# Performance work log

Measured on AMD Instinct MI355X. Metric: run time of the kernel, lower is better.

The kernel has to match this reference:

```python
import jax, jax.numpy as jnp
import numpy as np

N_NODES = 50000
N_EDGES = 800000
N_FEAT = 512
N_HEADS = 8
OUT_PER_HEAD = 32  # nhid // nheads = 256 // 8
ALPHA = 0.2  # LeakyReLU negative slope


def setup_inputs() -> dict:
    key = jax.random.key(0)
    ks = jax.random.split(key, 7)
    h = jax.random.normal(ks[0], (N_NODES, N_FEAT), dtype=jnp.float32)
    src = jax.random.randint(ks[1], (N_EDGES,), 0, N_NODES)
    dst = jax.random.randint(ks[2], (N_EDGES,), 0, N_NODES)
    # per-head linear W: [H, F, O], bias [H, O]; attention vector a: [H, 2O], bias [H]
    W = jax.random.normal(ks[3], (N_HEADS, N_FEAT, OUT_PER_HEAD), dtype=jnp.float32) * 0.05
    Wb = jax.random.normal(ks[4], (N_HEADS, OUT_PER_HEAD), dtype=jnp.float32) * 0.05
    a = jax.random.normal(ks[5], (N_HEADS, 2 * OUT_PER_HEAD), dtype=jnp.float32) * 0.05
    ab = jax.random.normal(ks[6], (N_HEADS,), dtype=jnp.float32) * 0.05
    return {"h": h, "src": src, "dst": dst, "W": W, "Wb": Wb, "a": a, "ab": ab}


def reference(h, src, dst, W, Wb, a, ab):
    N = h.shape[0]
    H, F_in, O = W.shape
    # Per-head projection Wh = W(h): [N, H, O]
    Wh = jnp.einsum('nf,hfo->nho', h, W) + Wb
    # a @ concat(Wh_src, Wh_dst) == a_src @ Wh_src + a_dst @ Wh_dst
    a_src, a_dst = a[:, :O], a[:, O:]
    e_s = jnp.einsum('nho,ho->nh', Wh, a_src)  # [N, H]
    e_d = jnp.einsum('nho,ho->nh', Wh, a_dst)
    e = e_s[src] + e_d[dst] + ab               # [E, H]
    e = jnp.where(e > 0, e, ALPHA * e)         # LeakyReLU
    # Segment softmax over incoming edges of each destination node
    m = jax.ops.segment_max(e, dst, num_segments=N)        # [N, H]
    m = jnp.where(jnp.isfinite(m), m, jnp.zeros_like(m))   # isolated nodes
    w = jnp.exp(e - m[dst])                                # [E, H]
    denom = jax.ops.segment_sum(w, dst, num_segments=N)    # [N, H]
    att = w / jnp.where(denom[dst] > 0, denom[dst], 1.0)   # [E, H]
    # Weighted aggregation of source projections, per head, then concat heads
    out = jax.ops.segment_sum(att[:, :, None] * Wh[src], dst, num_segments=N)  # [N, H, O]
    return out.reshape(N, H * O)
```

## Files before the change

### kernel.cpp

```cpp
#include <hip/hip_runtime.h>
#include <math.h>

#define ALPHA 0.2f
#define CAP 64

constexpr int F_IN  = 512;
constexpr int HO    = 256;
constexpr int NHEAD = 8;

using bf16x8 = __attribute__((ext_vector_type(8))) short;
using bf16x4 = __attribute__((ext_vector_type(4))) short;
using f32x4  = __attribute__((ext_vector_type(4))) float;

__device__ __forceinline__ ushort f2bf(float f) {
    uint u = __float_as_uint(f);
    uint r = (u + 0x7FFFu + ((u >> 16) & 1u)) >> 16;
    return (ushort)r;
}
__device__ __forceinline__ float bf2f(ushort b) {
    return __uint_as_float(((uint)b) << 16);
}

__global__ __launch_bounds__(256) void prep_kernel(const float* __restrict__ W,
                                                   ushort* __restrict__ Wf,
                                                   const int* __restrict__ dst,
                                                   int* __restrict__ cnt,
                                                   int* __restrict__ rnk, int E) {
    const int bid = blockIdx.x;
    const int t = threadIdx.x;
    if (bid < 64) {
        int g = bid * 256 + t;
        int l   = g & 63;
        int oct = (g >> 6) & 15;
        int ks  = g >> 10;
        int oc  = oct * 16 + (l & 15);
        int hh  = oc >> 5, oo = oc & 31;
        int kb  = ks * 32 + (l >> 4) * 8;
        ushort v[8];
#pragma unroll
        for (int j = 0; j < 8; ++j)
            v[j] = f2bf(W[((size_t)hh * F_IN + kb + j) * 32 + oo]);
        bf16x8 o = { (short)v[0], (short)v[1], (short)v[2], (short)v[3],
                     (short)v[4], (short)v[5], (short)v[6], (short)v[7] };
        *(bf16x8*)(Wf + (size_t)g * 8) = o;
    } else {
        int base = (bid - 64) * 1024;
#pragma unroll
        for (int q = 0; q < 4; ++q) {
            int i = base + q * 256 + t;
            if (i < E) rnk[i] = atomicAdd(&cnt[dst[i]], 1);
        }
    }
}

__global__ __launch_bounds__(256) void scan1_kernel(const int* __restrict__ cnt,
                                                    int* __restrict__ bsum, int N) {
    __shared__ int red[256];
    const int t = threadIdx.x;
    const int b0 = blockIdx.x * 1024;
    int s = 0;
#pragma unroll
    for (int q = 0; q < 4; ++q) {
        int i = b0 + t * 4 + q;
        if (i < N) s += cnt[i];
    }
    red[t] = s;
    __syncthreads();
    for (int st = 128; st > 0; st >>= 1) {
        if (t < st) red[t] += red[t + st];
        __syncthreads();
    }
    if (t == 0) bsum[blockIdx.x] = red[0];
}

__global__ __launch_bounds__(64) void scan2_kernel(int* __restrict__ bsum, int nblk) {
    int l = threadIdx.x;
    int x = (l < nblk) ? bsum[l] : 0;
    int inc = x;
    for (int d = 1; d < 64; d <<= 1) {
        int v = __shfl_up(inc, d);
        if (l >= d) inc += v;
    }
    if (l < nblk) bsum[l] = inc - x;
}

__global__ __launch_bounds__(256) void scan3_kernel(const int* __restrict__ cnt,
                                                    const int* __restrict__ bsum,
                                                    int* __restrict__ off, int N, int E) {
    __shared__ int part[256];
    const int t = threadIdx.x;
    const int b0 = blockIdx.x * 1024;
    int v[4];
    int s = 0;
#pragma unroll
    for (int q = 0; q < 4; ++q) {
        int i = b0 + t * 4 + q;
        v[q] = (i < N) ? cnt[i] : 0;
        s += v[q];
    }
    part[t] = s;
    __syncthreads();
    for (int d = 1; d < 256; d <<= 1) {
        int x = (t >= d) ? part[t - d] : 0;
        __syncthreads();
        part[t] += x;
        __syncthreads();
    }
    int run = bsum[blockIdx.x] + ((t == 0) ? 0 : part[t - 1]);
#pragma unroll
    for (int q = 0; q < 4; ++q) {
        int i = b0 + t * 4 + q;
        if (i < N) { off[i] = run; run += v[q]; }
    }
    if (blockIdx.x == 0 && t == 0) off[N] = E;
}

__global__ __launch_bounds__(256) void place_kernel(const int* __restrict__ src,
                                                    const int* __restrict__ dst,
                                                    const int* __restrict__ rnk,
                                                    const int* __restrict__ off,
                                                    int* __restrict__ se, int E) {
    int base = blockIdx.x * 1024;
#pragma unroll
    for (int q = 0; q < 4; ++q) {
        int i = base + q * 256 + threadIdx.x;
        if (i < E) se[off[dst[i]] + rnk[i]] = src[i];
    }
}

__global__ __launch_bounds__(256, 2) void gemm_kernel(
    const float* __restrict__ h, const ushort* __restrict__ Wf,
    const float* __restrict__ Wb, const float* __restrict__ a,
    ushort* __restrict__ Wh, float* __restrict__ es, float* __restrict__ ed, int N)
{
    __shared__ ushort hs[2][128 * 40];
    const int t = threadIdx.x;
    const int l = t & 63;
    const int w = t >> 6;
    const int l15 = l & 15, l4 = l >> 4;
    const int n0 = blockIdx.x * 128;

    const int sr = t >> 1;
    const int sc = (t & 1) * 16;
    int srow = n0 + sr; if (srow >= N) srow = N - 1;
    const float* hrow = h + (size_t)srow * F_IN + sc;

    f32x4 acc[4][8];
#pragma unroll
    for (int i = 0; i < 4; ++i)
#pragma unroll
        for (int nt = 0; nt < 8; ++nt) acc[i][nt] = (f32x4){0.f, 0.f, 0.f, 0.f};

    {
        float4 v0 = *(const float4*)(hrow);
        float4 v1 = *(const float4*)(hrow + 4);
        float4 v2 = *(const float4*)(hrow + 8);
        float4 v3 = *(const float4*)(hrow + 12);
        bf16x8 o0 = { (short)f2bf(v0.x), (short)f2bf(v0.y), (short)f2bf(v0.z), (short)f2bf(v0.w),
                      (short)f2bf(v1.x), (short)f2bf(v1.y), (short)f2bf(v1.z), (short)f2bf(v1.w) };
        bf16x8 o1 = { (short)f2bf(v2.x), (short)f2bf(v2.y), (short)f2bf(v2.z), (short)f2bf(v2.w),
                      (short)f2bf(v3.x), (short)f2bf(v3.y), (short)f2bf(v3.z), (short)f2bf(v3.w) };
        *(bf16x8*)&hs[0][sr * 40 + sc]     = o0;
        *(bf16x8*)&hs[0][sr * 40 + sc + 8] = o1;
    }
    __syncthreads();

    for (int ks = 0; ks < 16; ++ks) {
        const int cb = ks & 1;
        float4 nx0, nx1, nx2, nx3;
        if (ks < 15) {
            const float* p = hrow + (ks + 1) * 32;
            nx0 = *(const float4*)(p);
            nx1 = *(const float4*)(p + 4);
            nx2 = *(const float4*)(p + 8);
            nx3 = *(const float4*)(p + 12);
        }
        bf16x8 af[4];
#pragma unroll
        for (int i = 0; i < 4; ++i)
            af[i] = *(const bf16x8*)(Wf + ((size_t)((ks * 16 + 4 * w + i) * 64 + l)) * 8);
#pragma unroll
        for (int half = 0; half < 2; ++half) {
            bf16x8 b4[4];
#pragma unroll
            for (int j = 0; j < 4; ++j)
                b4[j] = *(const bf16x8*)&hs[cb][((half * 4 + j) * 16 + l15) * 40 + l4 * 8];
#pragma unroll
            for (int i = 0; i < 4; ++i)
#pragma unroll
                for (int j = 0; j < 4; ++j)
                    acc[i][half * 4 + j] = __builtin_amdgcn_mfma_f32_16x16x32_bf16(
                        af[i], b4[j], acc[i][half * 4 + j], 0, 0, 0);
        }
        if (ks < 15) {
            bf16x8 o0 = { (short)f2bf(nx0.x), (short)f2bf(nx0.y), (short)f2bf(nx0.z), (short)f2bf(nx0.w),
                          (short)f2bf(nx1.x), (short)f2bf(nx1.y), (short)f2bf(nx1.z), (short)f2bf(nx1.w) };
            bf16x8 o1 = { (short)f2bf(nx2.x), (short)f2bf(nx2.y), (short)f2bf(nx2.z), (short)f2bf(nx2.w),
                          (short)f2bf(nx3.x), (short)f2bf(nx3.y), (short)f2bf(nx3.z), (short)f2bf(nx3.w) };
            *(bf16x8*)&hs[cb ^ 1][sr * 40 + sc]     = o0;
            *(bf16x8*)&hs[cb ^ 1][sr * 40 + sc + 8] = o1;
            __syncthreads();
        }
    }

    float4 wb4[4], as4[4], ad4[4];
    int ocb[4];
#pragma unroll
    for (int i = 0; i < 4; ++i) {
        int oc_base = (4 * w + i) * 16 + (l4 << 2);
        ocb[i] = oc_base;
        int head = oc_base >> 5;
        wb4[i] = *(const float4*)(Wb + oc_base);
        as4[i] = *(const float4*)(a + head * 64 + (oc_base & 31));
        ad4[i] = *(const float4*)(a + head * 64 + 32 + (oc_base & 31));
    }
#pragma unroll
    for (int nt = 0; nt < 8; ++nt) {
        int node = n0 + nt * 16 + l15;
        bool ok = node < N;
        float pe[4] = {0.f, 0.f, 0.f, 0.f};
#pragma unroll
        for (int i = 0; i < 4; ++i) {
            f32x4 v = acc[i][nt];
            float r0 = v.x + wb4[i].x, r1 = v.y + wb4[i].y;
            float r2 = v.z + wb4[i].z, r3 = v.w + wb4[i].w;
            if (ok) {
                bf16x4 o = { (short)f2bf(r0), (short)f2bf(r1), (short)f2bf(r2), (short)f2bf(r3) };
                *(bf16x4*)(Wh + (size_t)node * HO + ocb[i]) = o;
            }
            float dsv = r0 * as4[i].x + r1 * as4[i].y + r2 * as4[i].z + r3 * as4[i].w;
            float ddv = r0 * ad4[i].x + r1 * ad4[i].y + r2 * ad4[i].z + r3 * ad4[i].w;
            int hp = i >> 1;
            pe[hp] += dsv; pe[2 + hp] += ddv;
        }
#pragma unroll
        for (int q = 0; q < 4; ++q) {
            pe[q] += __shfl_xor(pe[q], 16);
            pe[q] += __shfl_xor(pe[q], 32);
        }
        if (l4 == 0 && ok) {
            es[(size_t)node * NHEAD + 2 * w]     = pe[0];
            es[(size_t)node * NHEAD + 2 * w + 1] = pe[1];
            ed[(size_t)node * NHEAD + 2 * w]     = pe[2];
            ed[(size_t)node * NHEAD + 2 * w + 1] = pe[3];
        }
    }
}

__global__ __launch_bounds__(256) void node_kernel(
    const int* __restrict__ se, const int* __restrict__ off,
    const float* __restrict__ es, const float* __restrict__ ed,
    const float* __restrict__ ab, const ushort* __restrict__ Wh,
    float* __restrict__ out, int N)
{
    __shared__ float wbuf[4][CAP][NHEAD];
    __shared__ int   sbuf[4][CAP];
    __shared__ float dinv[4][NHEAD];

    const int t = threadIdx.x;
    const int l = t & 63;
    const int wv = t >> 6;
    const int n = blockIdx.x * 4 + wv;
    const bool active = n < N;

    int beg = 0, deg = 0;
    if (active) { beg = off[n]; deg = off[n + 1] - beg; }

    const int slot = l >> 3, hh = l & 7;
    float edn = 0.f, abh = 0.f;
    if (active && deg > 0) {
        edn = ed[(size_t)n * NHEAD + hh];
        abh = ab[hh];
    }

    float dloc = 0.f;
    for (int j = slot; j < deg; j += 8) {
        int s = se[beg + j];
        float ev = es[(size_t)s * NHEAD + hh] + edn + abh;
        ev = ev > 0.f ? ev : ALPHA * ev;
        float wj = __expf(ev);
        if (j < CAP) {
            wbuf[wv][j][hh] = wj;
            if (hh == 0) sbuf[wv][j] = s;
        }
        dloc += wj;
    }
    dloc += __shfl_xor(dloc, 8);
    dloc += __shfl_xor(dloc, 16);
    dloc += __shfl_xor(dloc, 32);
    if (slot == 0) dinv[wv][hh] = (dloc > 0.f) ? 1.f / dloc : 1.f;
    __syncthreads();

    const int oc0 = (l & 31) * 8;
    const int hb  = oc0 >> 5;
    const int par = l >> 5;
    float acc[8] = {0.f, 0.f, 0.f, 0.f, 0.f, 0.f, 0.f, 0.f};

    if (active) {
        const int dcap = deg < CAP ? deg : CAP;
        int j = par;
        for (; j + 6 < dcap; j += 8) {
            int s0 = sbuf[wv][j];
            int s1 = sbuf[wv][j + 2];
            int s2 = sbuf[wv][j + 4];
            int s3 = sbuf[wv][j + 6];
            float w0 = wbuf[wv][j][hb];
            float w1 = wbuf[wv][j + 2][hb];
            float w2 = wbuf[wv][j + 4][hb];
            float w3 = wbuf[wv][j + 6][hb];
            bf16x8 r0 = *(const bf16x8*)(Wh + (size_t)s0 * HO + oc0);
            bf16x8 r1 = *(const bf16x8*)(Wh + (size_t)s1 * HO + oc0);
            bf16x8 r2 = *(const bf16x8*)(Wh + (size_t)s2 * HO + oc0);
            bf16x8 r3 = *(const bf16x8*)(Wh + (size_t)s3 * HO + oc0);
#pragma unroll
            for (int i = 0; i < 8; ++i) acc[i] += w0 * bf2f((ushort)r0[i]);
#pragma unroll
            for (int i = 0; i < 8; ++i) acc[i] += w1 * bf2f((ushort)r1[i]);
#pragma unroll
            for (int i = 0; i < 8; ++i) acc[i] += w2 * bf2f((ushort)r2[i]);
#pragma unroll
            for (int i = 0; i < 8; ++i) acc[i] += w3 * bf2f((ushort)r3[i]);
        }
        for (; j < dcap; j += 2) {
            int s = sbuf[wv][j];
            float wj = wbuf[wv][j][hb];
            bf16x8 row = *(const bf16x8*)(Wh + (size_t)s * HO + oc0);
#pragma unroll
            for (int i = 0; i < 8; ++i)
                acc[i] += wj * bf2f((ushort)row[i]);
        }
        if (deg > CAP) {
            float edb = ed[(size_t)n * NHEAD + hb] + ab[hb];
            for (int j2 = CAP + par; j2 < deg; j2 += 2) {
                int s = se[beg + j2];
                float ev = es[(size_t)s * NHEAD + hb] + edb;
                ev = ev > 0.f ? ev : ALPHA * ev;
                float wj = __expf(ev);
                bf16x8 row = *(const bf16x8*)(Wh + (size_t)s * HO + oc0);
#pragma unroll
                for (int i = 0; i < 8; ++i)
                    acc[i] += wj * bf2f((ushort)row[i]);
            }
        }
    }
#pragma unroll
    for (int i = 0; i < 8; ++i) acc[i] += __shfl_xor(acc[i], 32);

    if (active && par == 0) {
        float inv = dinv[wv][hb];
        float4 o0 = make_float4(acc[0] * inv, acc[1] * inv, acc[2] * inv, acc[3] * inv);
        float4 o1 = make_float4(acc[4] * inv, acc[5] * inv, acc[6] * inv, acc[7] * inv);
        *(float4*)(out + (size_t)n * HO + oc0)     = o0;
        *(float4*)(out + (size_t)n * HO + oc0 + 4) = o1;
    }
}

extern "C" void kernel_launch(void* const* d_in, const int* in_sizes, int n_in,
                              void* d_out, int out_size, void* d_ws, size_t ws_size,
                              hipStream_t stream) {
    const float* h   = (const float*)d_in[0];
    const int*   src = (const int*)  d_in[1];
    const int*   dst = (const int*)  d_in[2];
    const float* W   = (const float*)d_in[3];
    const float* Wb  = (const float*)d_in[4];
    const float* a   = (const float*)d_in[5];
    const float* ab  = (const float*)d_in[6];
    float* out = (float*)d_out;

    const int N = in_sizes[0] / F_IN;
    const int E = in_sizes[1];

    auto align_up = [](size_t x) { return (x + 255) & ~size_t(255); };
    char* p = (char*)d_ws;
    ushort* Wh = (ushort*)p; p += align_up((size_t)N * HO * 2);
    float*  es = (float*)p;  p += align_up((size_t)N * NHEAD * 4);
    float*  ed = (float*)p;  p += align_up((size_t)N * NHEAD * 4);
    int* cnt   = (int*)p;    p += align_up((size_t)N * 4);
    int* off   = (int*)p;    p += align_up((size_t)(N + 1) * 4);
    int* rnk   = (int*)p;    p += align_up((size_t)E * 4);
    int* se    = (int*)p;    p += align_up((size_t)E * 4);
    int* bsum  = (int*)p;    p += align_up((size_t)64 * 4);
    ushort* Wf = (ushort*)p; p += align_up((size_t)16 * 16 * 64 * 8 * 2);

    const int nblk = (N + 1023) / 1024;
    const int EB   = (E + 1023) / 1024;
    const int GB   = (N + 127) / 128;

    hipMemsetAsync(cnt, 0, (size_t)N * sizeof(int), stream);
    prep_kernel<<<64 + EB, 256, 0, stream>>>(W, Wf, dst, cnt, rnk, E);
    scan1_kernel<<<nblk, 256, 0, stream>>>(cnt, bsum, N);
    scan2_kernel<<<1, 64, 0, stream>>>(bsum, nblk);
    scan3_kernel<<<nblk, 256, 0, stream>>>(cnt, bsum, off, N, E);
    place_kernel<<<EB, 256, 0, stream>>>(src, dst, rnk, off, se, E);
    gemm_kernel<<<GB, 256, 0, stream>>>(h, Wf, Wb, a, Wh, es, ed, N);
    node_kernel<<<(N + 3) / 4, 256, 0, stream>>>(se, off, es, ed, ab, Wh, out, N);
}
```

Baseline: 164.2 us.

## Sort destination nodes by in-degree so node kernel blocks are balanced

Builds a counting sort of nodes by in-degree (capped at 63) inside the existing scan kernels, using per-block histograms and a prefix over buckets. The result is a permutation that the node kernel uses to map waves to nodes, so the four waves in a block handle nodes of similar degree and fewer waves sit idle waiting on a long neighbour. It adds histogram atomics, one more scan step and an extra indirection per node. It also loses the locality of output writes, since consecutive waves no longer write adjacent rows.

```diff
diff --git a/kernel.cpp b/kernel.cpp
--- a/kernel.cpp
+++ b/kernel.cpp
@@ -7,6 +7,7 @@
 constexpr int F_IN  = 512;
 constexpr int HO    = 256;
 constexpr int NHEAD = 8;
+constexpr int MAXBLK = 64;
 
 using bf16x8 = __attribute__((ext_vector_type(8))) short;
 using bf16x4 = __attribute__((ext_vector_type(4))) short;
@@ -54,15 +55,24 @@
 }
 
 __global__ __launch_bounds__(256) void scan1_kernel(const int* __restrict__ cnt,
-                                                    int* __restrict__ bsum, int N) {
+                                                    int* __restrict__ bsum,
+                                                    int* __restrict__ bh,
+                                                    int N, int nblk) {
     __shared__ int red[256];
+    __shared__ int hb[64];
     const int t = threadIdx.x;
     const int b0 = blockIdx.x * 1024;
+    if (t < 64) hb[t] = 0;
+    __syncthreads();
     int s = 0;
 #pragma unroll
     for (int q = 0; q < 4; ++q) {
         int i = b0 + t * 4 + q;
-        if (i < N) s += cnt[i];
+        if (i < N) {
+            int v = cnt[i];
+            s += v;
+            atomicAdd(&hb[v > 63 ? 63 : v], 1);
+        }
     }
     red[t] = s;
     __syncthreads();
@@ -71,25 +81,50 @@
         __syncthreads();
     }
     if (t == 0) bsum[blockIdx.x] = red[0];
-}
-
-__global__ __launch_bounds__(64) void scan2_kernel(int* __restrict__ bsum, int nblk) {
-    int l = threadIdx.x;
-    int x = (l < nblk) ? bsum[l] : 0;
-    int inc = x;
-    for (int d = 1; d < 64; d <<= 1) {
-        int v = __shfl_up(inc, d);
-        if (l >= d) inc += v;
-    }
-    if (l < nblk) bsum[l] = inc - x;
+    if (t < 64) bh[t * nblk + blockIdx.x] = hb[t];
+}
+
+__global__ __launch_bounds__(128) void scan2_kernel(int* __restrict__ bsum, int nblk,
+                                                    const int* __restrict__ bh,
+                                                    int* __restrict__ obb) {
+    int t = threadIdx.x;
+    if (t < 64) {
+        int l = t;
+        int x = (l < nblk) ? bsum[l] : 0;
+        int inc = x;
+        for (int d = 1; d < 64; d <<= 1) {
+            int v = __shfl_up(inc, d);
+            if (l >= d) inc += v;
+        }
+        if (l < nblk) bsum[l] = inc - x;
+    } else {
+        int b = t - 64;
+        int tot = 0;
+        for (int k = 0; k < nblk; ++k) tot += bh[b * nblk + k];
+        int inc = tot;
+        for (int d = 1; d < 64; d <<= 1) {
+            int v = __shfl_up(inc, d);
+            if (b >= d) inc += v;
+        }
+        int run = inc - tot;
+        for (int k = 0; k < nblk; ++k) {
+            obb[b * nblk + k] = run;
+            run += bh[b * nblk + k];
+        }
+    }
 }
 
 __global__ __launch_bounds__(256) void scan3_kernel(const int* __restrict__ cnt,
                                                     const int* __restrict__ bsum,
-                                                    int* __restrict__ off, int N, int E) {
+                                                    int* __restrict__ off,
+                                                    const int* __restrict__ obb,
+                                                    int* __restrict__ perm,
+                                                    int N, int E, int nblk) {
     __shared__ int part[256];
+    __shared__ int hb[64];
     const int t = threadIdx.x;
     const int b0 = blockIdx.x * 1024;
+    if (t < 64) hb[t] = 0;
     int v[4];
     int s = 0;
 #pragma unroll
@@ -110,7 +145,12 @@
 #pragma unroll
     for (int q = 0; q < 4; ++q) {
         int i = b0 + t * 4 + q;
-        if (i < N) { off[i] = run; run += v[q]; }
+        if (i < N) {
+            off[i] = run; run += v[q];
+            int b = v[q] > 63 ? 63 : v[q];
+            int r = atomicAdd(&hb[b], 1);
+            perm[obb[b * nblk + blockIdx.x] + r] = i;
+        }
     }
     if (blockIdx.x == 0 && t == 0) off[N] = E;
 }
@@ -249,6 +289,7 @@
 
 __global__ __launch_bounds__(256) void node_kernel(
     const int* __restrict__ se, const int* __restrict__ off,
+    const int* __restrict__ perm,
     const float* __restrict__ es, const float* __restrict__ ed,
     const float* __restrict__ ab, const ushort* __restrict__ Wh,
     float* __restrict__ out, int N)
@@ -260,8 +301,9 @@
     const int t = threadIdx.x;
     const int l = t & 63;
     const int wv = t >> 6;
-    const int n = blockIdx.x * 4 + wv;
-    const bool active = n < N;
+    const int gi = blockIdx.x * 4 + wv;
+    const bool active = gi < N;
+    const int n = active ? perm[gi] : 0;
 
     int beg = 0, deg = 0;
     if (active) { beg = off[n]; deg = off[n + 1] - beg; }
@@ -379,7 +421,10 @@
     int* off   = (int*)p;    p += align_up((size_t)(N + 1) * 4);
     int* rnk   = (int*)p;    p += align_up((size_t)E * 4);
     int* se    = (int*)p;    p += align_up((size_t)E * 4);
-    int* bsum  = (int*)p;    p += align_up((size_t)64 * 4);
+    int* perm  = (int*)p;    p += align_up((size_t)N * 4);
+    int* bsum  = (int*)p;    p += align_up((size_t)MAXBLK * 4);
+    int* bh    = (int*)p;    p += align_up((size_t)64 * MAXBLK * 4);
+    int* obb   = (int*)p;    p += align_up((size_t)64 * MAXBLK * 4);
     ushort* Wf = (ushort*)p; p += align_up((size_t)16 * 16 * 64 * 8 * 2);
 
     const int nblk = (N + 1023) / 1024;
@@ -388,10 +433,10 @@
 
     hipMemsetAsync(cnt, 0, (size_t)N * sizeof(int), stream);
     prep_kernel<<<64 + EB, 256, 0, stream>>>(W, Wf, dst, cnt, rnk, E);
-    scan1_kernel<<<nblk, 256, 0, stream>>>(cnt, bsum, N);
-    scan2_kernel<<<1, 64, 0, stream>>>(bsum, nblk);
-    scan3_kernel<<<nblk, 256, 0, stream>>>(cnt, bsum, off, N, E);
+    scan1_kernel<<<nblk, 256, 0, stream>>>(cnt, bsum, bh, N, nblk);
+    scan2_kernel<<<1, 128, 0, stream>>>(bsum, nblk, bh, obb);
+    scan3_kernel<<<nblk, 256, 0, stream>>>(cnt, bsum, off, obb, perm, N, E, nblk);
     place_kernel<<<EB, 256, 0, stream>>>(src, dst, rnk, off, se, E);
     gemm_kernel<<<GB, 256, 0, stream>>>(h, Wf, Wb, a, Wh, es, ed, N);
-    node_kernel<<<(N + 3) / 4, 256, 0, stream>>>(se, off, es, ed, ab, Wh, out, N);
-}
+    node_kernel<<<(N + 3) / 4, 256, 0, stream>>>(se, off, perm, es, ed, ab, Wh, out, N);
+}
```

Result: slower. 177.9 us (+8.3%).
